# Kernel tuning notes

Hardware: AMD Instinct MI355X
Metric: run time of the kernel (lower is better)

## Reference

```python
import jax, jax.numpy as jnp
import numpy as np

N_HEAD = 8
D_HEAD = 64
D_MODEL = 512
CTX = 64
B = 2
Q_LEN = 2048
T = Q_LEN + CTX - 1


def setup_inputs() -> dict:
    key = jax.random.key(0)
    ks = jax.random.split(key, 7)
    HD = N_HEAD * D_HEAD
    return {
        "x": jax.random.normal(ks[0], (B, T, D_MODEL), jnp.float32),
        "r": jax.random.normal(ks[1], (CTX, D_MODEL), jnp.float32),
        "Wkv": jax.random.normal(ks[2], (D_MODEL, 2 * HD), jnp.float32) * 0.02,
        "Wq": jax.random.normal(ks[3], (D_MODEL, HD), jnp.float32) * 0.02,
        "bq": jax.random.normal(ks[4], (HD,), jnp.float32) * 0.02,
        "Wr": jax.random.normal(ks[5], (D_MODEL, HD), jnp.float32) * 0.02,
        "Wo": jax.random.normal(ks[6], (HD, D_MODEL), jnp.float32) * 0.02,
    }


def reference(x, r, Wkv, Wq, bq, Wr, Wo):
    Bb, Tt, _ = x.shape
    C = r.shape[0]
    H, Dh = N_HEAD, D_HEAD
    q_len = Tt - C + 1
    scale = Dh ** -0.5

    kv = x @ Wkv                                  # [B, T, 2*H*Dh]
    k_all = kv[..., : H * Dh].reshape(Bb, Tt, H, Dh)
    v_all = kv[..., H * Dh:].reshape(Bb, Tt, H, Dh)

    # sliding windows (torch unfold(1, ctx, 1) equivalent)
    idx = jnp.arange(q_len)[:, None] + jnp.arange(C)[None, :]   # [q, C]
    k_win = k_all[:, idx]                         # [B, q, C, H, Dh]
    v_win = v_all[:, idx]                         # [B, q, C, H, Dh]

    hq = (x[:, C - 1:] @ Wq + bq).reshape(Bb, q_len, H, Dh)     # [B, q, H, Dh]
    hr = (r @ Wr).reshape(C, H, Dh)                              # [C, H, Dh]

    # q . (k + r): split into content term + relative-position bias term
    scores = (jnp.einsum('bqhd,bqchd->bhqc', hq, k_win)
              + jnp.einsum('bqhd,chd->bhqc', hq, hr)) * scale    # [B, H, q, C]

    # padding mask: positions in first ctx-1 steps that are all-zero
    pad_mask = jnp.all(x[:, : C - 1] == 0, axis=-1)              # [B, C-1]
    full_mask = jnp.concatenate(
        [pad_mask, jnp.zeros((Bb, q_len), dtype=bool)], axis=1)  # [B, T]
    mask_win = full_mask[:, idx]                                 # [B, q, C]
    scores = jnp.where(mask_win[:, None], -jnp.inf, scores)

    w = jax.nn.softmax(scores, axis=-1)                          # [B, H, q, C]
    out = jnp.einsum('bhqc,bqchd->bqhd', w, v_win).reshape(Bb, q_len, H * Dh)
    return out @ Wo                                              # [B, q, d_model]
```

## Files before the change

### kernel.cpp

```cpp
#include <hip/hip_runtime.h>
#include <cstdint>
#include <cstddef>

#define NH 8
#define DH 64
#define DM 512
#define CTX 64
#define BB 2
#define QL 2048
#define TT (QL + CTX - 1)
#define HDIM 512
#define KVN 1024
#define KD 512

typedef unsigned short u16;
typedef __attribute__((ext_vector_type(8))) short bf16x8;
typedef __attribute__((ext_vector_type(4))) float f32x4;

__device__ __forceinline__ u16 f2bf(float f) {
    uint32_t u = __float_as_uint(f);
    u += 0x7FFF + ((u >> 16) & 1);
    return (u16)(u >> 16);
}

#define GLLDS(g, l) __builtin_amdgcn_global_load_lds( \
    (const __attribute__((address_space(1))) void*)(g), \
    (__attribute__((address_space(3))) void*)(l), 16, 0, 0)

__global__ __launch_bounds__(256) void prep_kernel(
    const float* __restrict__ x, const float* __restrict__ r,
    const float* __restrict__ Wkv, const float* __restrict__ Wq,
    const float* __restrict__ Wr, const float* __restrict__ Wo,
    u16* __restrict__ xb, u16* __restrict__ rb, u16* __restrict__ WkvqT,
    u16* __restrict__ WrT, u16* __restrict__ WoT, float* __restrict__ maskv)
{
    __shared__ float tile[64][65];
    __shared__ int anyflag;
    int bid = blockIdx.x;
    const int tid = threadIdx.x;

    if (bid < 2111) {
        int i = bid * 256 + tid;
        float4 v = ((const float4*)x)[i];
        ushort4 o; o.x = f2bf(v.x); o.y = f2bf(v.y); o.z = f2bf(v.z); o.w = f2bf(v.w);
        ((ushort4*)xb)[i] = o;
        return;
    }
    bid -= 2111;
    if (bid < 32) {
        int i = bid * 256 + tid;
        float4 v = ((const float4*)r)[i];
        ushort4 o; o.x = f2bf(v.x); o.y = f2bf(v.y); o.z = f2bf(v.z); o.w = f2bf(v.w);
        ((ushort4*)rb)[i] = o;
        return;
    }
    bid -= 32;
    if (bid >= 320) {
        int idx = bid - 320;
        int t = idx >> 1, b = idx & 1;
        const float* row = x + (size_t)(b * TT + t) * DM;
        bool nz = (row[tid] != 0.f) || (row[tid + 256] != 0.f);
        if (tid == 0) anyflag = 0;
        __syncthreads();
        unsigned long long bal = __ballot(nz);
        if ((tid & 63) == 0 && bal) atomicOr(&anyflag, 1);
        __syncthreads();
        if (tid == 0) maskv[b * 64 + t] = anyflag ? 0.f : -1e30f;
        return;
    }
    const float* W; u16* WT; int N; int tidx;
    if (bid < 128)      { W = Wkv; WT = WkvqT;                    N = 1024; tidx = bid; }
    else if (bid < 192) { W = Wq;  WT = WkvqT + (size_t)1024*512; N = 512;  tidx = bid - 128; }
    else if (bid < 256) { W = Wr;  WT = WrT;                      N = 512;  tidx = bid - 192; }
    else                { W = Wo;  WT = WoT;                      N = 512;  tidx = bid - 256; }
    const int tpr = N / 64;
    const int kb = (tidx / tpr) * 64, nb = (tidx % tpr) * 64;
    const int c4 = (tid & 15) * 4;
    for (int kk = tid >> 4; kk < 64; kk += 16) {
        float4 v = *(const float4*)&W[(size_t)(kb + kk) * N + nb + c4];
        tile[kk][c4 + 0] = v.x; tile[kk][c4 + 1] = v.y;
        tile[kk][c4 + 2] = v.z; tile[kk][c4 + 3] = v.w;
    }
    __syncthreads();
    for (int nn = tid >> 4; nn < 64; nn += 16) {
        ushort4 o;
        o.x = f2bf(tile[c4 + 0][nn]); o.y = f2bf(tile[c4 + 1][nn]);
        o.z = f2bf(tile[c4 + 2][nn]); o.w = f2bf(tile[c4 + 3][nn]);
        *(ushort4*)&WT[(size_t)(nb + nn) * KD + kb + c4] = o;
    }
}

__global__ __launch_bounds__(256) void gemm_fused(
    const u16* __restrict__ xb, const u16* __restrict__ WkvqT,
    u16* __restrict__ kvb, u16* __restrict__ hqb, const float* __restrict__ bq,
    const u16* __restrict__ rb, const u16* __restrict__ WrT,
    u16* __restrict__ hrb)
{
    __shared__ u16 As[2][128 * 32];
    __shared__ u16 Bs[2][128 * 32];

    const int tid  = threadIdx.x;
    const int lane = tid & 63;
    const int w    = tid >> 6;
    const int wm   = (w >> 1) * 64;
    const int wn   = (w & 1) * 64;

    const int bid = blockIdx.x;
    const bool g3 = (bid >= 396);
    const u16* A;  const u16* BT;
    int m0, n0;
    if (g3) { A = rb; BT = WrT;   m0 = 0;                n0 = (bid - 396) * 128; }
    else    { A = xb; BT = WkvqT; m0 = (bid / 12) * 128; n0 = (bid % 12) * 128; }

    const int am0 = tid >> 2;
    const int ak0 = (tid & 3) * 8;
    const u16* ga0 = A  + (size_t)(m0 + am0) * KD + ak0;
    const u16* ga1 = ga0 + (size_t)64 * KD;
    const u16* gb0 = BT + (size_t)(n0 + am0) * KD + ak0;
    const u16* gb1 = gb0 + (size_t)64 * KD;

#define STAGE_G1(buf, kt) do { \
    GLLDS(ga0 + (kt), &As[buf][(size_t)w * 512]); \
    GLLDS(ga1 + (kt), &As[buf][2048 + (size_t)w * 512]); \
    GLLDS(gb0 + (kt), &Bs[buf][(size_t)w * 512]); \
    GLLDS(gb1 + (kt), &Bs[buf][2048 + (size_t)w * 512]); \
} while (0)

    f32x4 acc[4][4];
#pragma unroll
    for (int i = 0; i < 4; i++)
#pragma unroll
        for (int j = 0; j < 4; j++)
            acc[i][j] = (f32x4){0.f, 0.f, 0.f, 0.f};

    STAGE_G1(0, 0);
    __syncthreads();

    int cur = 0;
    const int fm = lane & 15;
    const int fk = (lane >> 4) * 8;
    for (int kt = 0; kt < KD; kt += 32) {
        if (kt + 32 < KD) STAGE_G1(cur ^ 1, kt + 32);

        bf16x8 af[4], bfr[4];
#pragma unroll
        for (int i = 0; i < 4; i++)
            af[i] = *(const bf16x8*)&As[cur][(wm + i * 16 + fm) * 32 + fk];
#pragma unroll
        for (int j = 0; j < 4; j++)
            bfr[j] = *(const bf16x8*)&Bs[cur][(wn + j * 16 + fm) * 32 + fk];
#pragma unroll
        for (int i = 0; i < 4; i++)
#pragma unroll
            for (int j = 0; j < 4; j++)
                acc[i][j] = __builtin_amdgcn_mfma_f32_16x16x32_bf16(af[i], bfr[j], acc[i][j], 0, 0, 0);

        __syncthreads();
        cur ^= 1;
    }
#undef STAGE_G1

    const int fc = lane & 15;
    const int fr = (lane >> 4) * 4;
    if (!g3) {
        const bool iskv = (n0 < 1024);
#pragma unroll
        for (int i = 0; i < 4; i++)
#pragma unroll
            for (int rr = 0; rr < 4; rr++) {
                int row = m0 + wm + i * 16 + fr + rr;
                if (row < BB * TT) {
                    if (iskv) {
#pragma unroll
                        for (int j = 0; j < 4; j++) {
                            int col = n0 + wn + j * 16 + fc;
                            kvb[(size_t)row * KVN + col] = f2bf(acc[i][j][rr]);
                        }
                    } else {
                        int bb = row / TT;
                        int t  = row - bb * TT;
                        if (t >= CTX - 1) {
                            size_t orow = (size_t)(bb * QL + t - (CTX - 1));
#pragma unroll
                            for (int j = 0; j < 4; j++) {
                                int col = n0 + wn + j * 16 + fc - 1024;
                                hqb[orow * HDIM + col] = f2bf(acc[i][j][rr] + bq[col]);
                            }
                        }
                    }
                }
            }
    } else {
#pragma unroll
        for (int i = 0; i < 4; i++)
#pragma unroll
            for (int rr = 0; rr < 4; rr++) {
                int row = m0 + wm + i * 16 + fr + rr;
                if (row < CTX) {
#pragma unroll
                    for (int j = 0; j < 4; j++) {
                        int col = n0 + wn + j * 16 + fc;
                        hrb[(size_t)row * HDIM + col] = f2bf(acc[i][j][rr]);
                    }
                }
            }
    }
}

__global__ __launch_bounds__(256) void gemm_n64(
    const u16* __restrict__ A, const u16* __restrict__ BT,
    float* __restrict__ C, int M, int N)
{
    __shared__ u16 As[2][128 * 32];
    __shared__ u16 Bs[2][64 * 32];

    const int tid  = threadIdx.x;
    const int lane = tid & 63;
    const int w    = tid >> 6;
    const int wm   = (w >> 1) * 64;
    const int wn   = (w & 1) * 32;
    const int m0   = blockIdx.y * 128;
    const int n0   = blockIdx.x * 64;

    const int am0 = tid >> 2;
    const int ak0 = (tid & 3) * 8;
    const u16* ga0 = A  + (size_t)(m0 + am0) * KD + ak0;
    const u16* ga1 = ga0 + (size_t)64 * KD;
    const u16* gb0 = BT + (size_t)(n0 + am0) * KD + ak0;

#define STAGE_G2(buf, kt) do { \
    GLLDS(ga0 + (kt), &As[buf][(size_t)w * 512]); \
    GLLDS(ga1 + (kt), &As[buf][2048 + (size_t)w * 512]); \
    GLLDS(gb0 + (kt), &Bs[buf][(size_t)w * 512]); \
} while (0)

    f32x4 acc[4][2];
#pragma unroll
    for (int i = 0; i < 4; i++)
#pragma unroll
        for (int j = 0; j < 2; j++)
            acc[i][j] = (f32x4){0.f, 0.f, 0.f, 0.f};

    STAGE_G2(0, 0);
    __syncthreads();

    int cur = 0;
    const int fm = lane & 15;
    const int fk = (lane >> 4) * 8;
    for (int kt = 0; kt < KD; kt += 32) {
        if (kt + 32 < KD) STAGE_G2(cur ^ 1, kt + 32);

        bf16x8 af[4], bfr[2];
#pragma unroll
        for (int i = 0; i < 4; i++)
            af[i] = *(const bf16x8*)&As[cur][(wm + i * 16 + fm) * 32 + fk];
#pragma unroll
        for (int j = 0; j < 2; j++)
            bfr[j] = *(const bf16x8*)&Bs[cur][(wn + j * 16 + fm) * 32 + fk];
#pragma unroll
        for (int i = 0; i < 4; i++)
#pragma unroll
            for (int j = 0; j < 2; j++)
                acc[i][j] = __builtin_amdgcn_mfma_f32_16x16x32_bf16(af[i], bfr[j], acc[i][j], 0, 0, 0);

        __syncthreads();
        cur ^= 1;
    }
#undef STAGE_G2

    const int fc = lane & 15;
    const int fr = (lane >> 4) * 4;
#pragma unroll
    for (int i = 0; i < 4; i++)
#pragma unroll
        for (int rr = 0; rr < 4; rr++) {
            int row = m0 + wm + i * 16 + fr + rr;
            if (row < M) {
#pragma unroll
                for (int j = 0; j < 2; j++) {
                    int col = n0 + wn + j * 16 + fc;
                    C[(size_t)row * N + col] = acc[i][j][rr];
                }
            }
        }
}

__global__ __launch_bounds__(256) void attn_mfma(
    const u16* __restrict__ kvb, const u16* __restrict__ hqb,
    const u16* __restrict__ hrb, const float* __restrict__ maskv,
    u16* __restrict__ attnb)
{
    __shared__ __align__(16) char lds[55296];
    float* sprime = (float*)lds;
    u16*   vTs    = (u16*)(lds + 20480);
    u16*   wband  = (u16*)(lds + 37888);

    const int q0 = blockIdx.x * 64;
    const int h  = blockIdx.y;
    const int b  = blockIdx.z;
    const int tid  = threadIdx.x;
    const int lane = tid & 63;
    const int w    = tid >> 6;
    const int qb   = q0 + w * 16;

    const int vr0 = tid >> 4;
    const int vc4 = (tid & 15) * 4;
    ushort4 vreg[8];
#pragma unroll
    for (int i = 0; i < 8; i++) {
        int rr = vr0 + i * 16;
        if (rr < 127)
            vreg[i] = *(const ushort4*)&kvb[(size_t)(b * TT + q0 + rr) * KVN + HDIM + h * DH + vc4];
        else
            vreg[i] = (ushort4){0, 0, 0, 0};
    }

    {
        uint32_t* wz = (uint32_t*)wband;
#pragma unroll
        for (int i = 0; i < 17; i++) wz[tid + i * 256] = 0;
    }
    asm volatile("s_waitcnt lgkmcnt(0)" ::: "memory");
    __builtin_amdgcn_s_barrier();

    const int fm = lane & 15;
    const int fk = (lane >> 4) * 8;

    const u16* hqrow = hqb + (size_t)(b * QL + qb + fm) * HDIM + h * DH + fk;
    bf16x8 afr0 = *(const bf16x8*)(hqrow);
    bf16x8 afr1 = *(const bf16x8*)(hqrow + 32);

    {
        const u16* kbase = kvb + (size_t)(b * TT + qb + fm) * KVN + h * DH + fk;
#pragma unroll
        for (int nt = 0; nt < 5; nt++) {
            bf16x8 b0 = *(const bf16x8*)(kbase + (size_t)nt * 16 * KVN);
            bf16x8 b1 = *(const bf16x8*)(kbase + (size_t)nt * 16 * KVN + 32);
            f32x4 acc = (f32x4){0.f, 0.f, 0.f, 0.f};
            acc = __builtin_amdgcn_mfma_f32_16x16x32_bf16(afr0, b0, acc, 0, 0, 0);
            acc = __builtin_amdgcn_mfma_f32_16x16x32_bf16(afr1, b1, acc, 0, 0, 0);
            const int row = (lane >> 4) * 4;
#pragma unroll
            for (int r = 0; r < 4; r++)
                sprime[w * 1280 + (row + r) * 80 + nt * 16 + fm] = acc[r];
        }
    }
    {
        const u16* hrbase = hrb + (size_t)fm * HDIM + h * DH + fk;
#pragma unroll
        for (int nc = 0; nc < 4; nc++) {
            bf16x8 b0 = *(const bf16x8*)(hrbase + (size_t)nc * 16 * HDIM);
            bf16x8 b1 = *(const bf16x8*)(hrbase + (size_t)nc * 16 * HDIM + 32);
            f32x4 acc = (f32x4){0.f, 0.f, 0.f, 0.f};
            acc = __builtin_amdgcn_mfma_f32_16x16x32_bf16(afr0, b0, acc, 0, 0, 0);
            acc = __builtin_amdgcn_mfma_f32_16x16x32_bf16(afr1, b1, acc, 0, 0, 0);
            const int row = (lane >> 4) * 4;
#pragma unroll
            for (int r = 0; r < 4; r++)
                sprime[w * 1280 + (row + r) * 81 + nc * 16 + fm] += acc[r];
        }
    }

#pragma unroll
    for (int i = 0; i < 8; i++) {
        int rr = vr0 + i * 16;
        vTs[(vc4 + 0) * 136 + rr] = vreg[i].x;
        vTs[(vc4 + 1) * 136 + rr] = vreg[i].y;
        vTs[(vc4 + 2) * 136 + rr] = vreg[i].z;
        vTs[(vc4 + 3) * 136 + rr] = vreg[i].w;
    }

#pragma unroll 1
    for (int i = 0; i < 16; i++) {
        const int qloc = w * 16 + i;
        float s = sprime[w * 1280 + i * 81 + lane] * 0.125f;
        if (q0 == 0) {
            int t = qloc + lane;
            if (t < 63) s += maskv[b * 64 + t];
        }
        float mx = s;
#pragma unroll
        for (int off = 32; off; off >>= 1) mx = fmaxf(mx, __shfl_xor(mx, off, 64));
        float e = __expf(s - mx);
        float sum = e;
#pragma unroll
        for (int off = 32; off; off >>= 1) sum += __shfl_xor(sum, off, 64);
        wband[qloc * 136 + qloc + lane] = f2bf(e / sum);
    }
    __syncthreads();

    f32x4 oacc[4];
#pragma unroll
    for (int j = 0; j < 4; j++) oacc[j] = (f32x4){0.f, 0.f, 0.f, 0.f};
#pragma unroll
    for (int ks = 0; ks < 4; ks++) {
        bf16x8 wa = *(const bf16x8*)&wband[(w * 16 + fm) * 136 + ks * 32 + fk];
#pragma unroll
        for (int j = 0; j < 4; j++) {
            bf16x8 vb = *(const bf16x8*)&vTs[(j * 16 + fm) * 136 + ks * 32 + fk];
            oacc[j] = __builtin_amdgcn_mfma_f32_16x16x32_bf16(wa, vb, oacc[j], 0, 0, 0);
        }
    }
    {
        const int row = (lane >> 4) * 4;
#pragma unroll
        for (int j = 0; j < 4; j++)
#pragma unroll
            for (int r = 0; r < 4; r++)
                attnb[(size_t)(b * QL + qb + row + r) * HDIM + h * DH + j * 16 + fm] =
                    f2bf(oacc[j][r]);
    }
}

extern "C" void kernel_launch(void* const* d_in, const int* in_sizes, int n_in,
                              void* d_out, int out_size, void* d_ws, size_t ws_size,
                              hipStream_t stream)
{
    const float* x   = (const float*)d_in[0];
    const float* r   = (const float*)d_in[1];
    const float* Wkv = (const float*)d_in[2];
    const float* Wq  = (const float*)d_in[3];
    const float* bq  = (const float*)d_in[4];
    const float* Wr  = (const float*)d_in[5];
    const float* Wo  = (const float*)d_in[6];
    float* out = (float*)d_out;

    char* p = (char*)d_ws;
    u16* xb     = (u16*)p;  p += (size_t)4224 * 512 * 2;
    u16* rb     = (u16*)p;  p += (size_t)128 * 512 * 2;
    u16* WkvqT  = (u16*)p;  p += (size_t)1536 * 512 * 2;
    u16* WrT    = (u16*)p;  p += (size_t)512 * 512 * 2;
    u16* WoT    = (u16*)p;  p += (size_t)512 * 512 * 2;
    u16* kvb    = (u16*)p;  p += (size_t)4224 * 1024 * 2;
    u16* hqb    = (u16*)p;  p += (size_t)4096 * 512 * 2;
    u16* hrb    = (u16*)p;  p += (size_t)64 * 512 * 2;
    u16* attnb  = (u16*)p;  p += (size_t)4096 * 512 * 2;
    float* maskv = (float*)p;

    hipLaunchKernelGGL(prep_kernel, dim3(2589), dim3(256), 0, stream,
                       x, r, Wkv, Wq, Wr, Wo, xb, rb, WkvqT, WrT, WoT, maskv);
    hipLaunchKernelGGL(gemm_fused, dim3(400), dim3(256), 0, stream,
                       xb, WkvqT, kvb, hqb, bq, rb, WrT, hrb);
    hipLaunchKernelGGL(attn_mfma, dim3(QL / 64, NH, BB), dim3(256), 0, stream,
                       kvb, hqb, hrb, maskv, attnb);
    hipLaunchKernelGGL(gemm_n64, dim3(512 / 64, 4096 / 128), dim3(256), 0, stream,
                       attnb, WoT, out, 4096, 512);
}
```

Measured before the change: 124.8 us.

## Fuse fp32-to-bf16 conversion of x and r into projection GEMM A-loads

The separate prep pass that converted x and r to bf16 is removed. The projection GEMM now loads fp32 A tiles into registers, packs them to bf16 and writes them to LDS, with the next tile's load issued before the MFMAs. The padding-mask computation moves into extra blocks of the GEMM launch, so prep only transposes the weights. The softmax is also reworked so each wave handles 16 rows at once with 4 lanes per row instead of looping row by row. This saves a global round trip of the bf16 x copy, but the fp32 A reads now take a register-staged path instead of direct global-to-LDS loads and are twice as large.

```diff
diff --git a/kernel.cpp b/kernel.cpp
--- a/kernel.cpp
+++ b/kernel.cpp
@@ -22,52 +22,23 @@
     u += 0x7FFF + ((u >> 16) & 1);
     return (u16)(u >> 16);
 }
+__device__ __forceinline__ uint32_t packbf(float lo, float hi) {
+    return (uint32_t)f2bf(lo) | ((uint32_t)f2bf(hi) << 16);
+}
 
 #define GLLDS(g, l) __builtin_amdgcn_global_load_lds( \
     (const __attribute__((address_space(1))) void*)(g), \
     (__attribute__((address_space(3))) void*)(l), 16, 0, 0)
 
 __global__ __launch_bounds__(256) void prep_kernel(
-    const float* __restrict__ x, const float* __restrict__ r,
     const float* __restrict__ Wkv, const float* __restrict__ Wq,
     const float* __restrict__ Wr, const float* __restrict__ Wo,
-    u16* __restrict__ xb, u16* __restrict__ rb, u16* __restrict__ WkvqT,
-    u16* __restrict__ WrT, u16* __restrict__ WoT, float* __restrict__ maskv)
+    u16* __restrict__ WkvqT, u16* __restrict__ WrT, u16* __restrict__ WoT)
 {
     __shared__ float tile[64][65];
-    __shared__ int anyflag;
-    int bid = blockIdx.x;
+    const int bid = blockIdx.x;
     const int tid = threadIdx.x;
 
-    if (bid < 2111) {
-        int i = bid * 256 + tid;
-        float4 v = ((const float4*)x)[i];
-        ushort4 o; o.x = f2bf(v.x); o.y = f2bf(v.y); o.z = f2bf(v.z); o.w = f2bf(v.w);
-        ((ushort4*)xb)[i] = o;
-        return;
-    }
-    bid -= 2111;
-    if (bid < 32) {
-        int i = bid * 256 + tid;
-        float4 v = ((const float4*)r)[i];
-        ushort4 o; o.x = f2bf(v.x); o.y = f2bf(v.y); o.z = f2bf(v.z); o.w = f2bf(v.w);
-        ((ushort4*)rb)[i] = o;
-        return;
-    }
-    bid -= 32;
-    if (bid >= 320) {
-        int idx = bid - 320;
-        int t = idx >> 1, b = idx & 1;
-        const float* row = x + (size_t)(b * TT + t) * DM;
-        bool nz = (row[tid] != 0.f) || (row[tid + 256] != 0.f);
-        if (tid == 0) anyflag = 0;
-        __syncthreads();
-        unsigned long long bal = __ballot(nz);
-        if ((tid & 63) == 0 && bal) atomicOr(&anyflag, 1);
-        __syncthreads();
-        if (tid == 0) maskv[b * 64 + t] = anyflag ? 0.f : -1e30f;
-        return;
-    }
     const float* W; u16* WT; int N; int tidx;
     if (bid < 128)      { W = Wkv; WT = WkvqT;                    N = 1024; tidx = bid; }
     else if (bid < 192) { W = Wq;  WT = WkvqT + (size_t)1024*512; N = 512;  tidx = bid - 128; }
@@ -91,37 +62,67 @@
 }
 
 __global__ __launch_bounds__(256) void gemm_fused(
-    const u16* __restrict__ xb, const u16* __restrict__ WkvqT,
+    const float* __restrict__ x, const u16* __restrict__ WkvqT,
     u16* __restrict__ kvb, u16* __restrict__ hqb, const float* __restrict__ bq,
-    const u16* __restrict__ rb, const u16* __restrict__ WrT,
-    u16* __restrict__ hrb)
+    const float* __restrict__ r, const u16* __restrict__ WrT,
+    u16* __restrict__ hrb, float* __restrict__ maskv)
 {
-    __shared__ u16 As[2][128 * 32];
-    __shared__ u16 Bs[2][128 * 32];
-
-    const int tid  = threadIdx.x;
+    const int bid = blockIdx.x;
+    const int tid = threadIdx.x;
+
+    if (bid >= 400) {
+        __shared__ int anyflag;
+        int idx = bid - 400;
+        int t = idx >> 1, b = idx & 1;
+        const float* row = x + (size_t)(b * TT + t) * DM;
+        bool nz = (row[tid] != 0.f) || (row[tid + 256] != 0.f);
+        if (tid == 0) anyflag = 0;
+        __syncthreads();
+        unsigned long long bal = __ballot(nz);
+        if ((tid & 63) == 0 && bal) atomicOr(&anyflag, 1);
+        __syncthreads();
+        if (tid == 0) maskv[b * 64 + t] = anyflag ? 0.f : -1e30f;
+        return;
+    }
+
+    __shared__ __align__(16) u16 As[2][128 * 32];
+    __shared__ __align__(16) u16 Bs[2][128 * 32];
+
     const int lane = tid & 63;
     const int w    = tid >> 6;
     const int wm   = (w >> 1) * 64;
     const int wn   = (w & 1) * 64;
 
-    const int bid = blockIdx.x;
     const bool g3 = (bid >= 396);
-    const u16* A;  const u16* BT;
-    int m0, n0;
-    if (g3) { A = rb; BT = WrT;   m0 = 0;                n0 = (bid - 396) * 128; }
-    else    { A = xb; BT = WkvqT; m0 = (bid / 12) * 128; n0 = (bid % 12) * 128; }
+    const float* A; const u16* BT; int m0, n0, mrows;
+    if (g3) { A = r; BT = WrT;   m0 = 0;                n0 = (bid - 396) * 128; mrows = CTX; }
+    else    { A = x; BT = WkvqT; m0 = (bid / 12) * 128; n0 = (bid % 12) * 128;  mrows = BB * TT; }
+
+    const int arow = tid >> 1;
+    const int akh  = (tid & 1) * 16;
+    int grow = m0 + arow; if (grow >= mrows) grow = 0;
+    const float* gA = A + (size_t)grow * KD + akh;
 
     const int am0 = tid >> 2;
     const int ak0 = (tid & 3) * 8;
-    const u16* ga0 = A  + (size_t)(m0 + am0) * KD + ak0;
-    const u16* ga1 = ga0 + (size_t)64 * KD;
     const u16* gb0 = BT + (size_t)(n0 + am0) * KD + ak0;
     const u16* gb1 = gb0 + (size_t)64 * KD;
 
-#define STAGE_G1(buf, kt) do { \
-    GLLDS(ga0 + (kt), &As[buf][(size_t)w * 512]); \
-    GLLDS(ga1 + (kt), &As[buf][2048 + (size_t)w * 512]); \
+    float4 f0, f1, f2, f3;
+#define ALOAD(kt) do { \
+    f0 = *(const float4*)(gA + (kt));      f1 = *(const float4*)(gA + (kt) + 4); \
+    f2 = *(const float4*)(gA + (kt) + 8);  f3 = *(const float4*)(gA + (kt) + 12); \
+} while (0)
+#define AWRITE(buf) do { \
+    uint4 p0, p1; \
+    p0.x = packbf(f0.x, f0.y); p0.y = packbf(f0.z, f0.w); \
+    p0.z = packbf(f1.x, f1.y); p0.w = packbf(f1.z, f1.w); \
+    p1.x = packbf(f2.x, f2.y); p1.y = packbf(f2.z, f2.w); \
+    p1.z = packbf(f3.x, f3.y); p1.w = packbf(f3.z, f3.w); \
+    *(uint4*)&As[buf][arow * 32 + akh]     = p0; \
+    *(uint4*)&As[buf][arow * 32 + akh + 8] = p1; \
+} while (0)
+#define BSTAGE(buf, kt) do { \
     GLLDS(gb0 + (kt), &Bs[buf][(size_t)w * 512]); \
     GLLDS(gb1 + (kt), &Bs[buf][2048 + (size_t)w * 512]); \
 } while (0)
@@ -133,14 +134,17 @@
         for (int j = 0; j < 4; j++)
             acc[i][j] = (f32x4){0.f, 0.f, 0.f, 0.f};
 
-    STAGE_G1(0, 0);
+    ALOAD(0);
+    AWRITE(0);
+    BSTAGE(0, 0);
     __syncthreads();
 
     int cur = 0;
     const int fm = lane & 15;
     const int fk = (lane >> 4) * 8;
     for (int kt = 0; kt < KD; kt += 32) {
-        if (kt + 32 < KD) STAGE_G1(cur ^ 1, kt + 32);
+        const bool more = (kt + 32 < KD);
+        if (more) { ALOAD(kt + 32); BSTAGE(cur ^ 1, kt + 32); }
 
         bf16x8 af[4], bfr[4];
 #pragma unroll
@@ -155,10 +159,13 @@
             for (int j = 0; j < 4; j++)
                 acc[i][j] = __builtin_amdgcn_mfma_f32_16x16x32_bf16(af[i], bfr[j], acc[i][j], 0, 0, 0);
 
+        if (more) AWRITE(cur ^ 1);
         __syncthreads();
         cur ^= 1;
     }
-#undef STAGE_G1
+#undef ALOAD
+#undef AWRITE
+#undef BSTAGE
 
     const int fc = lane & 15;
     const int fr = (lane >> 4) * 4;
@@ -370,22 +377,35 @@
         vTs[(vc4 + 3) * 136 + rr] = vreg[i].w;
     }
 
-#pragma unroll 1
-    for (int i = 0; i < 16; i++) {
+    {
+        const int i  = lane >> 2;
+        const int g  = lane & 3;
         const int qloc = w * 16 + i;
-        float s = sprime[w * 1280 + i * 81 + lane] * 0.125f;
+        const float* srow = &sprime[w * 1280 + i * 81 + g * 16];
+        float sv[16];
+#pragma unroll
+        for (int j = 0; j < 16; j++) sv[j] = srow[j] * 0.125f;
         if (q0 == 0) {
-            int t = qloc + lane;
-            if (t < 63) s += maskv[b * 64 + t];
+#pragma unroll
+            for (int j = 0; j < 16; j++) {
+                int t = qloc + g * 16 + j;
+                if (t < 63) sv[j] += maskv[b * 64 + t];
+            }
         }
-        float mx = s;
-#pragma unroll
-        for (int off = 32; off; off >>= 1) mx = fmaxf(mx, __shfl_xor(mx, off, 64));
-        float e = __expf(s - mx);
-        float sum = e;
-#pragma unroll
-        for (int off = 32; off; off >>= 1) sum += __shfl_xor(sum, off, 64);
-        wband[qloc * 136 + qloc + lane] = f2bf(e / sum);
+        float mx = sv[0];
+#pragma unroll
+        for (int j = 1; j < 16; j++) mx = fmaxf(mx, sv[j]);
+        mx = fmaxf(mx, __shfl_xor(mx, 1, 64));
+        mx = fmaxf(mx, __shfl_xor(mx, 2, 64));
+        float sum = 0.f;
+#pragma unroll
+        for (int j = 0; j < 16; j++) { sv[j] = __expf(sv[j] - mx); sum += sv[j]; }
+        sum += __shfl_xor(sum, 1, 64);
+        sum += __shfl_xor(sum, 2, 64);
+        float inv = 1.f / sum;
+        u16* wrow = &wband[qloc * 136 + qloc + g * 16];
+#pragma unroll
+        for (int j = 0; j < 16; j++) wrow[j] = f2bf(sv[j] * inv);
     }
     __syncthreads();
 
@@ -426,8 +446,6 @@
     float* out = (float*)d_out;
 
     char* p = (char*)d_ws;
-    u16* xb     = (u16*)p;  p += (size_t)4224 * 512 * 2;
-    u16* rb     = (u16*)p;  p += (size_t)128 * 512 * 2;
     u16* WkvqT  = (u16*)p;  p += (size_t)1536 * 512 * 2;
     u16* WrT    = (u16*)p;  p += (size_t)512 * 512 * 2;
     u16* WoT    = (u16*)p;  p += (size_t)512 * 512 * 2;
@@ -437,10 +455,10 @@
     u16* attnb  = (u16*)p;  p += (size_t)4096 * 512 * 2;
     float* maskv = (float*)p;
 
-    hipLaunchKernelGGL(prep_kernel, dim3(2589), dim3(256), 0, stream,
-                       x, r, Wkv, Wq, Wr, Wo, xb, rb, WkvqT, WrT, WoT, maskv);
-    hipLaunchKernelGGL(gemm_fused, dim3(400), dim3(256), 0, stream,
-                       xb, WkvqT, kvb, hqb, bq, rb, WrT, hrb);
+    hipLaunchKernelGGL(prep_kernel, dim3(320), dim3(256), 0, stream,
+                       Wkv, Wq, Wr, Wo, WkvqT, WrT, WoT);
+    hipLaunchKernelGGL(gemm_fused, dim3(528), dim3(256), 0, stream,
+                       x, WkvqT, kvb, hqb, bq, r, WrT, hrb, maskv);
     hipLaunchKernelGGL(attn_mfma, dim3(QL / 64, NH, BB), dim3(256), 0, stream,
                        kvb, hqb, hrb, maskv, attnb);
     hipLaunchKernelGGL(gemm_n64, dim3(512 / 64, 4096 / 128), dim3(256), 0, stream,
```

After: 125.4 us. No clear change (+0.5%).
